# Performance work log

Hardware: AMD Instinct MI355X
Metric: run time of the kernel (lower is better)

## Reference

```python
import jax, jax.numpy as jnp
import numpy as np

DIM = 1024
H = 16
D = DIM // H  # head_dim = 64
SCALE = 1.0 / np.sqrt(D)


def setup_inputs() -> dict:
    key = jax.random.key(0)
    ks = jax.random.split(key, 4)
    B, S = 4, 4096
    std = 1.0 / np.sqrt(DIM)
    return {
        "x": jax.random.normal(ks[0], (B, S, DIM), jnp.float32),
        "Wqkv": jax.random.normal(ks[1], (DIM, 3 * DIM), jnp.float32) * std,
        "bqkv": jnp.zeros((3 * DIM,), jnp.float32),
        "Wq": jax.random.normal(ks[2], (DIM, DIM), jnp.float32) * std,
        "bq": jnp.zeros((DIM,), jnp.float32),
        "Wproj": jax.random.normal(ks[3], (DIM, DIM), jnp.float32) * std,
        "bproj": jnp.zeros((DIM,), jnp.float32),
        "num_anchor_tokens": 512,
    }


def reference(x, Wqkv, bqkv, Wq, bq, Wproj, bproj, num_anchor_tokens):
    B, S, _ = x.shape
    A = num_anchor_tokens  # static Python int
    anchors = x[:, :A, :]          # (B, A, DIM)
    queries = x[:, A:, :]          # (B, Q, DIM)
    Q = S - A

    # Anchor tokens: full qkv projection
    qkv = anchors @ Wqkv + bqkv                      # (B, A, 3*DIM)
    qkv = qkv.reshape(B, A, 3, H, D)
    aq = jnp.transpose(qkv[:, :, 0], (0, 2, 1, 3))   # (B, H, A, D)
    ak = jnp.transpose(qkv[:, :, 1], (0, 2, 1, 3))   # (B, H, A, D)
    av = jnp.transpose(qkv[:, :, 2], (0, 2, 1, 3))   # (B, H, A, D)

    # Query tokens: query-only projection
    qq = (queries @ Wq + bq).reshape(B, Q, H, D)
    qq = jnp.transpose(qq, (0, 2, 1, 3))             # (B, H, Q, D)

    q_all = jnp.concatenate([aq, qq], axis=2)        # (B, H, S, D)

    # Everyone attends only to anchor keys/values
    scores = jnp.einsum("bhsd,bhad->bhsa", q_all, ak) * SCALE  # (B, H, S, A)
    attn = jax.nn.softmax(scores, axis=-1)
    out = jnp.einsum("bhsa,bhad->bhsd", attn, av)    # (B, H, S, D)
    out = jnp.transpose(out, (0, 2, 1, 3)).reshape(B, S, DIM)
    return out @ Wproj + bproj
```

## Files before the change

kernel.cpp:

```cpp
#include <hip/hip_runtime.h>
#include <hip/hip_bf16.h>

#define DIMC 1024
#define HC   16
#define DC   64
#define BC   4
#define SC   4096
#define ANC  512
#define QNC  3584
#define GK   1024
#define QSCALE (0.125f * 1.44269504088896f)

typedef __attribute__((ext_vector_type(4))) float f32x4;
typedef __attribute__((ext_vector_type(8))) short s16x8;
typedef __attribute__((ext_vector_type(4))) short s16x4;

__device__ inline short f2bf(float f) {
    unsigned u = __builtin_bit_cast(unsigned, f);
    u += 0x7fff + ((u >> 16) & 1);
    return (short)(u >> 16);
}
__device__ inline unsigned cvtpk(float lo, float hi) {
    unsigned d;
    asm("v_cvt_pk_bf16_f32 %0, %1, %2" : "=v"(d) : "v"(lo), "v"(hi));
    return d;
}

#define GLOAD16(gp, lp) __builtin_amdgcn_global_load_lds( \
    (const __attribute__((address_space(1))) void*)(gp),  \
    (__attribute__((address_space(3))) void*)(lp), 16, 0, 0)

__global__ __launch_bounds__(256) void cast_f32_bf16(
    const float* __restrict__ in, short* __restrict__ out, int n4)
{
    int i = blockIdx.x * blockDim.x + threadIdx.x;
    const int stride = gridDim.x * blockDim.x;
    for (; i < n4; i += stride) {
        float4 v = ((const float4*)in)[i];
        s16x4 o = { f2bf(v.x), f2bf(v.y), f2bf(v.z), f2bf(v.w) };
        ((s16x4*)out)[i] = o;
    }
}

__global__ __launch_bounds__(256) void transpose_cast(
    const float* __restrict__ W, short* __restrict__ Wt, int K, int N)
{
    __shared__ float t[32][33];
    const int tx = threadIdx.x & 31, ty = threadIdx.x >> 5;
    const int nt = blockIdx.x * 32, kt = blockIdx.y * 32;
    #pragma unroll
    for (int j = 0; j < 4; ++j)
        t[ty + 8 * j][tx] = W[(size_t)(kt + ty + 8 * j) * N + nt + tx];
    __syncthreads();
    #pragma unroll
    for (int j = 0; j < 4; ++j)
        Wt[(size_t)(nt + ty + 8 * j) * K + kt + tx] = f2bf(t[tx][ty + 8 * j]);
}

__global__ __launch_bounds__(256) void transpose_cast2(
    const float* __restrict__ W0, short* __restrict__ Wt0,
    const float* __restrict__ W1, short* __restrict__ Wt1)
{
    __shared__ float t[32][33];
    const float* W = blockIdx.z ? W1 : W0;
    short* Wt = blockIdx.z ? Wt1 : Wt0;
    const int tx = threadIdx.x & 31, ty = threadIdx.x >> 5;
    const int nt = blockIdx.x * 32, kt = blockIdx.y * 32;
    #pragma unroll
    for (int j = 0; j < 4; ++j)
        t[ty + 8 * j][tx] = W[(size_t)(kt + ty + 8 * j) * 1024 + nt + tx];
    __syncthreads();
    #pragma unroll
    for (int j = 0; j < 4; ++j)
        Wt[(size_t)(nt + ty + 8 * j) * 1024 + kt + tx] = f2bf(t[tx][ty + 8 * j]);
}

__device__ __forceinline__ void gemm_body(
    short* Als, short* Bls,
    const char* Arow0, const char* Brow0, const float* bias,
    float* outF, short* outQ, short* outK, short* outVt,
    int bm, int bn, int bb, int blocal, int rowOff, int mode)
{
    const int tid = threadIdx.x;
    const int wave = tid >> 6, lane = tid & 63;
    const int q = lane & 15, g = lane >> 4;
    const int wm = wave >> 1, wn = wave & 1;

    int srcOff[4], dstOff[4];
    #pragma unroll
    for (int p = 0; p < 4; ++p) {
        const int ca = p * 256 + tid;
        const int row = ca >> 3;
        const int cc = (ca & 7) ^ (row & 7);
        srcOff[p] = row * (GK * 2) + cc * 16;
        dstOff[p] = ca * 16;
    }

    f32x4 acc[4][4];
    #pragma unroll
    for (int i = 0; i < 4; ++i)
        #pragma unroll
        for (int j = 0; j < 4; ++j) acc[i][j] = (f32x4){0.f, 0.f, 0.f, 0.f};

    const int q7 = q & 7;

    for (int k0 = 0; k0 < GK; k0 += 64) {
        const int kb = k0 * 2;
        #pragma unroll
        for (int p = 0; p < 4; ++p)
            GLOAD16(Arow0 + srcOff[p] + kb, (char*)Als + dstOff[p]);
        #pragma unroll
        for (int p = 0; p < 4; ++p)
            GLOAD16(Brow0 + srcOff[p] + kb, (char*)Bls + dstOff[p]);
        __syncthreads();

        #pragma unroll
        for (int kk = 0; kk < 2; ++kk) {
            const int rc = ((kk * 4 + g) ^ q7) << 4;
            s16x8 aF[4], bF[4];
            #pragma unroll
            for (int mi = 0; mi < 4; ++mi)
                aF[mi] = *(const s16x8*)((const char*)Als +
                         (wm * 64 + mi * 16 + q) * 128 + rc);
            #pragma unroll
            for (int ni = 0; ni < 4; ++ni)
                bF[ni] = *(const s16x8*)((const char*)Bls +
                         (wn * 64 + ni * 16 + q) * 128 + rc);
            #pragma unroll
            for (int mi = 0; mi < 4; ++mi)
                #pragma unroll
                for (int ni = 0; ni < 4; ++ni)
                    acc[mi][ni] = __builtin_amdgcn_mfma_f32_16x16x32_bf16(
                        aF[mi], bF[ni], acc[mi][ni], 0, 0, 0);
        }
        __syncthreads();
    }

    #pragma unroll
    for (int ni = 0; ni < 4; ++ni) {
        const int col = bn + wn * 64 + ni * 16 + q;
        const float bv = bias[col];
        #pragma unroll
        for (int mi = 0; mi < 4; ++mi) {
            const int rl0 = blocal + wm * 64 + mi * 16 + 4 * g;
            #pragma unroll
            for (int r = 0; r < 4; ++r) {
                const int rl = rl0 + r;
                const float v = acc[mi][ni][r] + bv;
                if (mode == 2) {
                    outF[(size_t)(bm + wm * 64 + mi * 16 + 4 * g + r) * 1024 + col] = v;
                } else if (mode == 1) {
                    const int h = col >> 6, d = col & 63;
                    outQ[(((size_t)(bb * HC + h)) * SC + rowOff + rl) * DC + d] =
                        f2bf(v * QSCALE);
                } else {
                    const int which = col >> 10;
                    const int hd = col & 1023;
                    const int h = hd >> 6, d = hd & 63;
                    const size_t bh = (size_t)(bb * HC + h);
                    if (which == 0)
                        outQ[(bh * SC + rl) * DC + d] = f2bf(v * QSCALE);
                    else if (which == 1)
                        outK[(bh * ANC + rl) * DC + d] = f2bf(v);
                    else
                        outVt[(bh * DC + d) * ANC + rl] = f2bf(v);
                }
            }
        }
    }
}

__global__ __launch_bounds__(256) void gemm_k1k2(
    const short* __restrict__ xb,
    const short* __restrict__ Wqkvt, const float* __restrict__ bqkv,
    const short* __restrict__ Wqt,   const float* __restrict__ bq,
    short* __restrict__ Qb, short* __restrict__ Kb, short* __restrict__ Vtb)
{
    __shared__ __align__(16) short Als[128 * 64];
    __shared__ __align__(16) short Bls[128 * 64];

    const int i = blockIdx.x;
    const char* Arow0; const char* Brow0; const float* bias;
    int bm, bn, bb, blocal, rowOff, mode;
    if (i < 384) {
        const int c = i & 7, j = i >> 3;
        bn = (j % 24) * 128;
        bm = ((j / 24) * 8 + c) * 128;
        bb = bm / ANC; blocal = bm % ANC; rowOff = 0; mode = 0;
        Arow0 = (const char*)(xb + ((size_t)bb * SC + blocal) * GK);
        Brow0 = (const char*)(Wqkvt + (size_t)bn * GK);
        bias = bqkv;
    } else {
        const int i2 = i - 384;
        const int c = i2 & 7, j = i2 >> 3;
        bn = (j % 8) * 128;
        bm = ((j / 8) * 8 + c) * 128;
        bb = bm / QNC; blocal = bm % QNC; rowOff = ANC; mode = 1;
        Arow0 = (const char*)(xb + ((size_t)bb * SC + ANC + blocal) * GK);
        Brow0 = (const char*)(Wqt + (size_t)bn * GK);
        bias = bq;
    }
    gemm_body(Als, Bls, Arow0, Brow0, bias,
              nullptr, Qb, Kb, Vtb, bm, bn, bb, blocal, rowOff, mode);
}

__global__ __launch_bounds__(256) void gemm_proj(
    const short* __restrict__ Abase, const short* __restrict__ Bt,
    const float* __restrict__ bias, float* __restrict__ outF)
{
    __shared__ __align__(16) short Als[128 * 64];
    __shared__ __align__(16) short Bls[128 * 64];

    const int i = blockIdx.x;
    const int c = i & 7, j = i >> 3;
    const int bn = (j % 8) * 128;
    const int bm = ((j / 8) * 8 + c) * 128;
    const char* Arow0 = (const char*)(Abase + (size_t)bm * GK);
    const char* Brow0 = (const char*)(Bt + (size_t)bn * GK);
    gemm_body(Als, Bls, Arow0, Brow0, bias,
              outF, nullptr, nullptr, nullptr, bm, bn, 0, bm, 0, 2);
}

__global__ __launch_bounds__(512, 2) void attn_mfma(
    const short* __restrict__ Qb,
    const short* __restrict__ Kb,
    const short* __restrict__ Vtb,
    short* __restrict__ Aout)
{
    __shared__ __align__(16) char lds[147456];

    const int tid = threadIdx.x;
    const int wave = tid >> 6, lane = tid & 63;
    const int q = lane & 15, g = lane >> 4;
    const int q7 = q & 7;
    const int G = g ^ q7;
    const int bh = blockIdx.x >> 2;
    const int qc = blockIdx.x & 3;
    const int sbase = qc * 1024 + wave * 128;

    {
        const char* src = (const char*)(Kb + (size_t)bh * ANC * DC);
        #pragma unroll
        for (int l = 0; l < 8; ++l) {
            int i = l * 512 + tid;
            int row = i >> 3, cg = i & 7;
            union { float4 v; unsigned long long d[2]; } u;
            u.v = *(const float4*)(src + (size_t)i * 16);
            int kk = cg >> 2;
            int u0 = (2 * cg) & 7;
            int pc0 = 4 * kk + (u0 & 3);
            int hh = (u0 >> 2) << 3;
            int r7 = row & 7;
            char* dst = lds + row * 128;
            *(unsigned long long*)(dst + ((pc0 ^ r7) << 4) + hh) = u.d[0];
            *(unsigned long long*)(dst + (((pc0 + 1) ^ r7) << 4) + hh) = u.d[1];
        }
    }
    {
        const char* src = (const char*)(Vtb + (size_t)bh * DC * ANC);
        #pragma unroll
        for (int l = 0; l < 8; ++l) {
            int i = l * 512 + tid;
            int row = i >> 6, cg = i & 63;
            union { float4 v; unsigned long long d[2]; } u;
            u.v = *(const float4*)(src + (size_t)i * 16);
            int t2 = cg >> 2;
            int u0 = (2 * cg) & 7;
            int pc0 = 4 * t2 + (u0 & 3);
            int hh = (u0 >> 2) << 3;
            int r7 = row & 7;
            char* dst = lds + 65536 + row * 1024;
            *(unsigned long long*)(dst + ((pc0 ^ r7) << 4) + hh) = u.d[0];
            *(unsigned long long*)(dst + (((pc0 + 1) ^ r7) << 4) + hh) = u.d[1];
        }
    }
    __syncthreads();

    char* slot = lds + 131072 + wave * 2048;
    const int srow = lane >> 2, sc2 = lane & 3;
    const int sr7 = srow & 7;

    const int cgA = 2 * sc2, kkA = cgA >> 2, u0A = (2 * cgA) & 7;
    const int pcA = 4 * kkA + (u0A & 3), hA = (u0A >> 2) << 3;
    const int cgB = cgA + 1, kkB = cgB >> 2, u0B = (2 * cgB) & 7;
    const int pcB = 4 * kkB + (u0B & 3), hB = (u0B >> 2) << 3;
    const int wA0 = srow * 128 + ((pcA ^ sr7) << 4) + hA;
    const int wA1 = srow * 128 + (((pcA + 1) ^ sr7) << 4) + hA;
    const int wB0 = srow * 128 + ((pcB ^ sr7) << 4) + hB;
    const int wB1 = srow * 128 + (((pcB + 1) ^ sr7) << 4) + hB;
    const int wb0 = srow * 128 + (((sc2 * 2 + 0) ^ sr7) << 4);
    const int wb1 = srow * 128 + (((sc2 * 2 + 1) ^ sr7) << 4);
    const int sw = q7 << 4;

    const int off0 = G << 4, off1 = off0 ^ 64;
    const char* kb0 = lds + q * 128 + off0;
    const char* kb1 = lds + q * 128 + off1;
    const char* vregion = lds + 65536;
    const unsigned vo0 = (unsigned)((q +  0) * 1024 + off0);
    const unsigned vo1 = (unsigned)((q + 16) * 1024 + off0);
    const unsigned vo2 = (unsigned)((q + 32) * 1024 + off0);
    const unsigned vo3 = (unsigned)((q + 48) * 1024 + off0);

    const size_t qrow0 = (size_t)bh * SC;

    union { float4 v; unsigned long long d[2]; } gqA0, gqA1, gqB0, gqB1;
    {
        const char* QA = (const char*)(Qb + (qrow0 + sbase) * DC);
        gqA0.v = *(const float4*)(QA + lane * 32);
        gqA1.v = *(const float4*)(QA + lane * 32 + 16);
        const char* QB = QA + 16 * DC * 2;
        gqB0.v = *(const float4*)(QB + lane * 32);
        gqB1.v = *(const float4*)(QB + lane * 32 + 16);
    }

    for (int tp = 0; tp < 4; ++tp) {
        const int s0A = sbase + tp * 32;
        const int s0B = s0A + 16;

        *(unsigned long long*)(slot + wA0) = gqA0.d[0];
        *(unsigned long long*)(slot + wA1) = gqA0.d[1];
        *(unsigned long long*)(slot + wB0) = gqA1.d[0];
        *(unsigned long long*)(slot + wB1) = gqA1.d[1];
        __asm__ __volatile__("" ::: "memory");
        s16x8 qfA0 = *(const s16x8*)(slot + q * 128 + off0);
        s16x8 qfA1 = *(const s16x8*)(slot + q * 128 + off1);
        __asm__ __volatile__("" ::: "memory");
        *(unsigned long long*)(slot + wA0) = gqB0.d[0];
        *(unsigned long long*)(slot + wA1) = gqB0.d[1];
        *(unsigned long long*)(slot + wB0) = gqB1.d[0];
        *(unsigned long long*)(slot + wB1) = gqB1.d[1];
        __asm__ __volatile__("" ::: "memory");
        s16x8 qfB0 = *(const s16x8*)(slot + q * 128 + off0);
        s16x8 qfB1 = *(const s16x8*)(slot + q * 128 + off1);

        s16x8 pfA[16], pfB[16];
        float psA0 = 0.f, psA1 = 0.f, psA2 = 0.f, psA3 = 0.f;
        float psB0 = 0.f, psB1 = 0.f, psB2 = 0.f, psB3 = 0.f;
        __builtin_amdgcn_s_setprio(1);
        #pragma unroll
        for (int t2 = 0; t2 < 16; ++t2) {
            const int be = (2 * t2) * 2048, bo = be + 2048;
            s16x8 kfe0 = *(const s16x8*)(kb0 + be);
            s16x8 kfe1 = *(const s16x8*)(kb1 + be);
            f32x4 sA = (f32x4){0.f, 0.f, 0.f, 0.f};
            sA = __builtin_amdgcn_mfma_f32_16x16x32_bf16(kfe0, qfA0, sA, 0, 0, 0);
            sA = __builtin_amdgcn_mfma_f32_16x16x32_bf16(kfe1, qfA1, sA, 0, 0, 0);
            f32x4 sB = (f32x4){0.f, 0.f, 0.f, 0.f};
            sB = __builtin_amdgcn_mfma_f32_16x16x32_bf16(kfe0, qfB0, sB, 0, 0, 0);
            sB = __builtin_amdgcn_mfma_f32_16x16x32_bf16(kfe1, qfB1, sB, 0, 0, 0);
            s16x8 kfo0 = *(const s16x8*)(kb0 + bo);
            s16x8 kfo1 = *(const s16x8*)(kb1 + bo);
            f32x4 tA = (f32x4){0.f, 0.f, 0.f, 0.f};
            tA = __builtin_amdgcn_mfma_f32_16x16x32_bf16(kfo0, qfA0, tA, 0, 0, 0);
            tA = __builtin_amdgcn_mfma_f32_16x16x32_bf16(kfo1, qfA1, tA, 0, 0, 0);
            f32x4 tB = (f32x4){0.f, 0.f, 0.f, 0.f};
            tB = __builtin_amdgcn_mfma_f32_16x16x32_bf16(kfo0, qfB0, tB, 0, 0, 0);
            tB = __builtin_amdgcn_mfma_f32_16x16x32_bf16(kfo1, qfB1, tB, 0, 0, 0);

            float eA0 = exp2f(sA[0]), eA1 = exp2f(sA[1]);
            float eA2 = exp2f(sA[2]), eA3 = exp2f(sA[3]);
            float fA0 = exp2f(tA[0]), fA1 = exp2f(tA[1]);
            float fA2 = exp2f(tA[2]), fA3 = exp2f(tA[3]);
            psA0 += eA0 + fA0; psA1 += eA1 + fA1;
            psA2 += eA2 + fA2; psA3 += eA3 + fA3;
            float eB0 = exp2f(sB[0]), eB1 = exp2f(sB[1]);
            float eB2 = exp2f(sB[2]), eB3 = exp2f(sB[3]);
            float fB0 = exp2f(tB[0]), fB1 = exp2f(tB[1]);
            float fB2 = exp2f(tB[2]), fB3 = exp2f(tB[3]);
            psB0 += eB0 + fB0; psB1 += eB1 + fB1;
            psB2 += eB2 + fB2; psB3 += eB3 + fB3;

            union { s16x8 v; unsigned u[4]; } pkA, pkB;
            pkA.u[0] = cvtpk(eA0, eA1); pkA.u[1] = cvtpk(eA2, eA3);
            pkA.u[2] = cvtpk(fA0, fA1); pkA.u[3] = cvtpk(fA2, fA3);
            pfA[t2] = pkA.v;
            pkB.u[0] = cvtpk(eB0, eB1); pkB.u[1] = cvtpk(eB2, eB3);
            pkB.u[2] = cvtpk(fB0, fB1); pkB.u[3] = cvtpk(fB2, fB3);
            pfB[t2] = pkB.v;
        }
        __builtin_amdgcn_s_setprio(0);

        {
            const int snext = (tp < 3) ? (s0A + 32) : sbase;
            const char* QA = (const char*)(Qb + (qrow0 + snext) * DC);
            gqA0.v = *(const float4*)(QA + lane * 32);
            gqA1.v = *(const float4*)(QA + lane * 32 + 16);
            const char* QB = QA + 16 * DC * 2;
            gqB0.v = *(const float4*)(QB + lane * 32);
            gqB1.v = *(const float4*)(QB + lane * 32 + 16);
            __asm__ __volatile__("" :
                "+v"(gqA0.v.x), "+v"(gqA0.v.y), "+v"(gqA0.v.z), "+v"(gqA0.v.w),
                "+v"(gqA1.v.x), "+v"(gqA1.v.y), "+v"(gqA1.v.z), "+v"(gqA1.v.w),
                "+v"(gqB0.v.x), "+v"(gqB0.v.y), "+v"(gqB0.v.z), "+v"(gqB0.v.w),
                "+v"(gqB1.v.x), "+v"(gqB1.v.y), "+v"(gqB1.v.z), "+v"(gqB1.v.w));
        }

        float sumA = (psA0 + psA1) + (psA2 + psA3);
        sumA += __shfl_xor(sumA, 16);
        sumA += __shfl_xor(sumA, 32);
        const float rinvA = 1.0f / sumA;
        float sumB = (psB0 + psB1) + (psB2 + psB3);
        sumB += __shfl_xor(sumB, 16);
        sumB += __shfl_xor(sumB, 32);
        const float rinvB = 1.0f / sumB;

        f32x4 oaccA[4], oaccB[4];
        #pragma unroll
        for (int md = 0; md < 4; ++md) {
            oaccA[md] = (f32x4){0.f, 0.f, 0.f, 0.f};
            oaccB[md] = (f32x4){0.f, 0.f, 0.f, 0.f};
        }
        __builtin_amdgcn_s_setprio(1);
        #pragma unroll
        for (int t2 = 0; t2 < 16; ++t2) {
            const unsigned tx = (unsigned)(t2 << 6);
            s16x8 vf0 = *(const s16x8*)(vregion + (vo0 ^ tx));
            oaccA[0] = __builtin_amdgcn_mfma_f32_16x16x32_bf16(vf0, pfA[t2], oaccA[0], 0, 0, 0);
            oaccB[0] = __builtin_amdgcn_mfma_f32_16x16x32_bf16(vf0, pfB[t2], oaccB[0], 0, 0, 0);
            s16x8 vf1 = *(const s16x8*)(vregion + (vo1 ^ tx));
            oaccA[1] = __builtin_amdgcn_mfma_f32_16x16x32_bf16(vf1, pfA[t2], oaccA[1], 0, 0, 0);
            oaccB[1] = __builtin_amdgcn_mfma_f32_16x16x32_bf16(vf1, pfB[t2], oaccB[1], 0, 0, 0);
            s16x8 vf2 = *(const s16x8*)(vregion + (vo2 ^ tx));
            oaccA[2] = __builtin_amdgcn_mfma_f32_16x16x32_bf16(vf2, pfA[t2], oaccA[2], 0, 0, 0);
            oaccB[2] = __builtin_amdgcn_mfma_f32_16x16x32_bf16(vf2, pfB[t2], oaccB[2], 0, 0, 0);
            s16x8 vf3 = *(const s16x8*)(vregion + (vo3 ^ tx));
            oaccA[3] = __builtin_amdgcn_mfma_f32_16x16x32_bf16(vf3, pfA[t2], oaccA[3], 0, 0, 0);
            oaccB[3] = __builtin_amdgcn_mfma_f32_16x16x32_bf16(vf3, pfB[t2], oaccB[3], 0, 0, 0);
        }
        __builtin_amdgcn_s_setprio(0);

        __asm__ __volatile__("" ::: "memory");
        #pragma unroll
        for (int md = 0; md < 4; ++md) {
            union { unsigned long long d; unsigned u[2]; } ow;
            ow.u[0] = cvtpk(oaccA[md][0] * rinvA, oaccA[md][1] * rinvA);
            ow.u[1] = cvtpk(oaccA[md][2] * rinvA, oaccA[md][3] * rinvA);
            *(unsigned long long*)(slot + q * 128 + ((32 * md + 8 * g) ^ sw)) = ow.d;
        }
        __asm__ __volatile__("" ::: "memory");
        {
            float4 o0 = *(const float4*)(slot + wb0);
            float4 o1 = *(const float4*)(slot + wb1);
            char* Op = (char*)Aout +
                (((size_t)(bh >> 4) * SC + s0A + srow) * DIMC + (bh & 15) * DC) * 2 +
                sc2 * 32;
            *(float4*)(Op) = o0;
            *(float4*)(Op + 16) = o1;
        }
        __asm__ __volatile__("" ::: "memory");
        #pragma unroll
        for (int md = 0; md < 4; ++md) {
            union { unsigned long long d; unsigned u[2]; } ow;
            ow.u[0] = cvtpk(oaccB[md][0] * rinvB, oaccB[md][1] * rinvB);
            ow.u[1] = cvtpk(oaccB[md][2] * rinvB, oaccB[md][3] * rinvB);
            *(unsigned long long*)(slot + q * 128 + ((32 * md + 8 * g) ^ sw)) = ow.d;
        }
        __asm__ __volatile__("" ::: "memory");
        {
            float4 o0 = *(const float4*)(slot + wb0);
            float4 o1 = *(const float4*)(slot + wb1);
            char* Op = (char*)Aout +
                (((size_t)(bh >> 4) * SC + s0B + srow) * DIMC + (bh & 15) * DC) * 2 +
                sc2 * 32;
            *(float4*)(Op) = o0;
            *(float4*)(Op + 16) = o1;
        }
    }
}

extern "C" void kernel_launch(void* const* d_in, const int* in_sizes, int n_in,
                              void* d_out, int out_size, void* d_ws, size_t ws_size,
                              hipStream_t stream)
{
    (void)in_sizes; (void)n_in; (void)out_size; (void)ws_size;

    const float* x     = (const float*)d_in[0];
    const float* Wqkv  = (const float*)d_in[1];
    const float* bqkv  = (const float*)d_in[2];
    const float* Wq    = (const float*)d_in[3];
    const float* bq    = (const float*)d_in[4];
    const float* Wproj = (const float*)d_in[5];
    const float* bproj = (const float*)d_in[6];

    short* xb = (short*)d_out;
    short* Qb = xb + (size_t)16777216;
    short* Kb     = (short*)d_ws;
    short* Vtb    = Kb  + (size_t)2097152;
    short* Ab     = Vtb + (size_t)2097152;
    short* Wqkvt  = Ab  + (size_t)16777216;
    short* Wqt    = Wqkvt + (size_t)3145728;
    short* Wprojt = Wqt   + (size_t)1048576;

    cast_f32_bf16<<<dim3(2048), dim3(256), 0, stream>>>(x, xb, 16777216 / 4);
    transpose_cast<<<dim3(96, 32), dim3(256), 0, stream>>>(Wqkv, Wqkvt, 1024, 3072);
    transpose_cast2<<<dim3(32, 32, 2), dim3(256), 0, stream>>>(Wq, Wqt, Wproj, Wprojt);

    gemm_k1k2<<<dim3(1280), dim3(256), 0, stream>>>(
        xb, Wqkvt, bqkv, Wqt, bq, Qb, Kb, Vtb);

    attn_mfma<<<dim3(256), dim3(512), 0, stream>>>(Qb, Kb, Vtb, Ab);

    gemm_proj<<<dim3(1024), dim3(256), 0, stream>>>(Ab, Wprojt, bproj, (float*)d_out);
}
```

Before: 194.1 us.

## Fuse cast/transpose prepasses into one launch and double attention waves per block

The three preprocessing kernels (x cast to bf16 and the two weight transpose-casts) are merged into one launch that dispatches on block index, removing two kernel launches and their gaps. The attention kernel moves from 512 to 1024 threads per block, with each wave handling 64 query rows instead of 128. K/V staging into LDS is split across twice as many threads, and the per-wave Q staging slots grow the LDS allocation to 160KB. This aims to hide latency with more waves, but doubles the VGPR pressure per CU under the new launch bounds, and launch_bounds(1024,4) may be unreachable given the LDS size.

```diff
diff --git a/kernel.cpp b/kernel.cpp
--- a/kernel.cpp
+++ b/kernel.cpp
@@ -30,24 +30,12 @@
     (const __attribute__((address_space(1))) void*)(gp),  \
     (__attribute__((address_space(3))) void*)(lp), 16, 0, 0)
 
-__global__ __launch_bounds__(256) void cast_f32_bf16(
-    const float* __restrict__ in, short* __restrict__ out, int n4)
-{
-    int i = blockIdx.x * blockDim.x + threadIdx.x;
-    const int stride = gridDim.x * blockDim.x;
-    for (; i < n4; i += stride) {
-        float4 v = ((const float4*)in)[i];
-        s16x4 o = { f2bf(v.x), f2bf(v.y), f2bf(v.z), f2bf(v.w) };
-        ((s16x4*)out)[i] = o;
-    }
-}
-
-__global__ __launch_bounds__(256) void transpose_cast(
-    const float* __restrict__ W, short* __restrict__ Wt, int K, int N)
-{
-    __shared__ float t[32][33];
+__device__ __forceinline__ void tc_tile(
+    const float* __restrict__ W, short* __restrict__ Wt, int K, int N,
+    int bx, int by, float (*t)[33])
+{
     const int tx = threadIdx.x & 31, ty = threadIdx.x >> 5;
-    const int nt = blockIdx.x * 32, kt = blockIdx.y * 32;
+    const int nt = bx * 32, kt = by * 32;
     #pragma unroll
     for (int j = 0; j < 4; ++j)
         t[ty + 8 * j][tx] = W[(size_t)(kt + ty + 8 * j) * N + nt + tx];
@@ -57,22 +45,31 @@
         Wt[(size_t)(nt + ty + 8 * j) * K + kt + tx] = f2bf(t[tx][ty + 8 * j]);
 }
 
-__global__ __launch_bounds__(256) void transpose_cast2(
-    const float* __restrict__ W0, short* __restrict__ Wt0,
-    const float* __restrict__ W1, short* __restrict__ Wt1)
+__global__ __launch_bounds__(256) void prepass(
+    const float* __restrict__ x, short* __restrict__ xb,
+    const float* __restrict__ Wqkv, short* __restrict__ Wqkvt,
+    const float* __restrict__ Wq, short* __restrict__ Wqt,
+    const float* __restrict__ Wproj, short* __restrict__ Wprojt)
 {
     __shared__ float t[32][33];
-    const float* W = blockIdx.z ? W1 : W0;
-    short* Wt = blockIdx.z ? Wt1 : Wt0;
-    const int tx = threadIdx.x & 31, ty = threadIdx.x >> 5;
-    const int nt = blockIdx.x * 32, kt = blockIdx.y * 32;
-    #pragma unroll
-    for (int j = 0; j < 4; ++j)
-        t[ty + 8 * j][tx] = W[(size_t)(kt + ty + 8 * j) * 1024 + nt + tx];
-    __syncthreads();
-    #pragma unroll
-    for (int j = 0; j < 4; ++j)
-        Wt[(size_t)(nt + ty + 8 * j) * 1024 + kt + tx] = f2bf(t[tx][ty + 8 * j]);
+    const int b = blockIdx.x;
+    if (b < 2048) {
+        int i = b * 256 + threadIdx.x;
+        for (; i < 4194304; i += 2048 * 256) {
+            float4 v = ((const float4*)x)[i];
+            s16x4 o = { f2bf(v.x), f2bf(v.y), f2bf(v.z), f2bf(v.w) };
+            ((s16x4*)xb)[i] = o;
+        }
+    } else if (b < 5120) {
+        const int z = b - 2048;
+        tc_tile(Wqkv, Wqkvt, 1024, 3072, z % 96, z / 96, t);
+    } else {
+        const int z = b - 5120;
+        const float* W = (z < 1024) ? Wq : Wproj;
+        short* Wt = (z < 1024) ? Wqt : Wprojt;
+        const int zz = z & 1023;
+        tc_tile(W, Wt, 1024, 1024, zz & 31, zz >> 5, t);
+    }
 }
 
 __device__ __forceinline__ void gemm_body(
@@ -221,13 +218,13 @@
               outF, nullptr, nullptr, nullptr, bm, bn, 0, bm, 0, 2);
 }
 
-__global__ __launch_bounds__(512, 2) void attn_mfma(
+__global__ __launch_bounds__(1024, 4) void attn_mfma(
     const short* __restrict__ Qb,
     const short* __restrict__ Kb,
     const short* __restrict__ Vtb,
     short* __restrict__ Aout)
 {
-    __shared__ __align__(16) char lds[147456];
+    __shared__ __align__(16) char lds[163840];
 
     const int tid = threadIdx.x;
     const int wave = tid >> 6, lane = tid & 63;
@@ -236,13 +233,13 @@
     const int G = g ^ q7;
     const int bh = blockIdx.x >> 2;
     const int qc = blockIdx.x & 3;
-    const int sbase = qc * 1024 + wave * 128;
+    const int sbase = qc * 1024 + wave * 64;
 
     {
         const char* src = (const char*)(Kb + (size_t)bh * ANC * DC);
         #pragma unroll
-        for (int l = 0; l < 8; ++l) {
-            int i = l * 512 + tid;
+        for (int l = 0; l < 4; ++l) {
+            int i = l * 1024 + tid;
             int row = i >> 3, cg = i & 7;
             union { float4 v; unsigned long long d[2]; } u;
             u.v = *(const float4*)(src + (size_t)i * 16);
@@ -259,8 +256,8 @@
     {
         const char* src = (const char*)(Vtb + (size_t)bh * DC * ANC);
         #pragma unroll
-        for (int l = 0; l < 8; ++l) {
-            int i = l * 512 + tid;
+        for (int l = 0; l < 4; ++l) {
+            int i = l * 1024 + tid;
             int row = i >> 6, cg = i & 63;
             union { float4 v; unsigned long long d[2]; } u;
             u.v = *(const float4*)(src + (size_t)i * 16);
@@ -313,7 +310,7 @@
         gqB1.v = *(const float4*)(QB + lane * 32 + 16);
     }
 
-    for (int tp = 0; tp < 4; ++tp) {
+    for (int tp = 0; tp < 2; ++tp) {
         const int s0A = sbase + tp * 32;
         const int s0B = s0A + 16;
 
@@ -381,7 +378,7 @@
         __builtin_amdgcn_s_setprio(0);
 
         {
-            const int snext = (tp < 3) ? (s0A + 32) : sbase;
+            const int snext = (tp < 1) ? (s0A + 32) : sbase;
             const char* QA = (const char*)(Qb + (qrow0 + snext) * DC);
             gqA0.v = *(const float4*)(QA + lane * 32);
             gqA1.v = *(const float4*)(QA + lane * 32 + 16);
@@ -491,14 +488,13 @@
     short* Wqt    = Wqkvt + (size_t)3145728;
     short* Wprojt = Wqt   + (size_t)1048576;
 
-    cast_f32_bf16<<<dim3(2048), dim3(256), 0, stream>>>(x, xb, 16777216 / 4);
-    transpose_cast<<<dim3(96, 32), dim3(256), 0, stream>>>(Wqkv, Wqkvt, 1024, 3072);
-    transpose_cast2<<<dim3(32, 32, 2), dim3(256), 0, stream>>>(Wq, Wqt, Wproj, Wprojt);
+    prepass<<<dim3(7168), dim3(256), 0, stream>>>(
+        x, xb, Wqkv, Wqkvt, Wq, Wqt, Wproj, Wprojt);
 
     gemm_k1k2<<<dim3(1280), dim3(256), 0, stream>>>(
         xb, Wqkvt, bqkv, Wqt, bq, Qb, Kb, Vtb);
 
-    attn_mfma<<<dim3(256), dim3(512), 0, stream>>>(Qb, Kb, Vtb, Ab);
+    attn_mfma<<<dim3(256), dim3(1024), 0, stream>>>(Qb, Kb, Vtb, Ab);
 
     gemm_proj<<<dim3(1024), dim3(256), 0, stream>>>(Ab, Wprojt, bproj, (float*)d_out);
 }
```

New measurement: 240.7 us. 1.24x slower.
